# Kernel tuning notes

Measured on AMD Instinct MI355X. Metric: run time of the kernel, lower is better.

The kernel has to match this reference:

```python
import jax, jax.numpy as jnp
import numpy as np

N, T, D, H = 128, 64, 1024, 1024
DA = 4  # spatial dim of feature map


def setup_inputs() -> dict:
    key = jax.random.key(0)
    k1, k2, k3, k4, k5 = jax.random.split(key, 5)
    x = jax.random.normal(k1, (N, T, D), dtype=jnp.float32)
    A = jax.random.normal(k2, (N, H, DA, DA), dtype=jnp.float32)
    Wx = jax.random.normal(k3, (D, 4 * H), dtype=jnp.float32) / np.sqrt(D)
    Wh = jax.random.normal(k4, (H, 4 * H), dtype=jnp.float32) / np.sqrt(H)
    Wattn = jax.random.normal(k5, (H, 4 * H), dtype=jnp.float32) / np.sqrt(H)
    b = jnp.zeros((4 * H,), dtype=jnp.float32)
    return {"x": x, "A": A, "Wx": Wx, "Wh": Wh, "Wattn": Wattn, "b": b}


def _dot_product_attention(prev_h, A_flat):
    # prev_h: (N, H), A_flat: (N, H, L) with L = DA*DA
    scores = jnp.einsum('nh,nhl->nl', prev_h, A_flat) / jnp.sqrt(jnp.float32(H))
    w = jax.nn.softmax(scores, axis=-1)              # (N, L)
    attn = jnp.einsum('nhl,nl->nh', A_flat, w)       # (N, H)
    return attn


def reference(x, A, Wx, Wh, Wattn, b):
    A_flat = A.reshape(A.shape[0], A.shape[1], -1)   # (N, H, L)
    h0 = A.mean(axis=(2, 3))                          # (N, H)
    c0 = h0
    x_t = jnp.swapaxes(x, 0, 1)                       # (T, N, D)

    def step(carry, xt):
        h, c = carry
        attn = _dot_product_attention(h, A_flat)
        a = xt @ Wx + h @ Wh + attn @ Wattn + b       # (N, 4H)
        i, f, o, g = jnp.split(a, 4, axis=1)
        i = jax.nn.sigmoid(i)
        f = jax.nn.sigmoid(f)
        o = jax.nn.sigmoid(o)
        g = jnp.tanh(g)
        c_next = f * c + i * g
        h_next = o * jnp.tanh(c_next)
        return (h_next, c_next), h_next

    _, hn = jax.lax.scan(step, (h0, c0), x_t)         # hn: (T, N, H)
    return jnp.swapaxes(hn, 0, 1)                      # (N, T, H)
```

## Files before the change

### kernel.cpp

```cpp
#include <hip/hip_runtime.h>
#include <stdint.h>
#include <math.h>

typedef __attribute__((ext_vector_type(8))) short short8;
typedef __attribute__((ext_vector_type(4))) short short4v;
typedef __attribute__((ext_vector_type(4))) float f32x4;

__device__ __forceinline__ short f2bf(float f){
  union { float f; uint32_t u; } x; x.f = f;
  uint32_t r = x.u + 0x7fffu + ((x.u >> 16) & 1u);
  return (short)(r >> 16);
}
__device__ __forceinline__ float bf2f(short s){
  union { uint32_t u; float f; } x; x.u = ((uint32_t)(uint16_t)s) << 16;
  return x.f;
}

__device__ __forceinline__ unsigned ld_llc_u32(const void* p){
  return __hip_atomic_load((const unsigned*)p, __ATOMIC_RELAXED, __HIP_MEMORY_SCOPE_AGENT);
}
__device__ __forceinline__ void st_llc_u32(void* p, unsigned v){
  __hip_atomic_store((unsigned*)p, v, __ATOMIC_RELAXED, __HIP_MEMORY_SCOPE_AGENT);
}


__global__ __launch_bounds__(256) void k_wt(const float* __restrict__ Wx,
                                            const float* __restrict__ Wh,
                                            const float* __restrict__ Wattn,
                                            short* __restrict__ W3T){
  __shared__ float tile[64][65];
  int bk = blockIdx.x % 48, bj = blockIdx.x / 48;
  int tx = threadIdx.x & 63, ty = threadIdx.x >> 6;
  int k0 = bk * 64, j0 = bj * 64;
  #pragma unroll
  for (int i = 0; i < 16; ++i){
    int kk = ty * 16 + i;
    int k = k0 + kk;
    const float* src = (k < 1024) ? (Wx + (size_t)k * 4096)
                     : (k < 2048) ? (Wh + (size_t)(k - 1024) * 4096)
                                  : (Wattn + (size_t)(k - 2048) * 4096);
    tile[kk][tx] = src[j0 + tx];
  }
  __syncthreads();
  #pragma unroll
  for (int i = 0; i < 16; ++i){
    int jj = ty * 16 + i;
    W3T[(size_t)(j0 + jj) * 3072 + k0 + tx] = f2bf(tile[tx][jj]);
  }
}

__global__ __launch_bounds__(256) void k_cast(const float* __restrict__ in,
                                              short* __restrict__ out, int n4){
  int i = blockIdx.x * 256 + threadIdx.x;
  if (i >= n4) return;
  float4 v = ((const float4*)in)[i];
  short4v o; o[0] = f2bf(v.x); o[1] = f2bf(v.y); o[2] = f2bf(v.z); o[3] = f2bf(v.w);
  *(short4v*)(out + (size_t)i * 4) = o;
}

__global__ __launch_bounds__(256) void k_castA(const float* __restrict__ A,
                                               short* __restrict__ Abf,
                                               short* __restrict__ Atr){
  const int n = blockIdx.x;
  const int tid = threadIdx.x;
  __shared__ short tile[256][17];
  for (int it = 0; it < 4; ++it){
    int h = it * 256 + tid;
    const float* src = A + ((size_t)n * 1024 + h) * 16;
    short o[16];
    #pragma unroll
    for (int l = 0; l < 16; ++l) o[l] = f2bf(src[l]);
    short8 p0, p1;
    #pragma unroll
    for (int l = 0; l < 8; ++l){ p0[l] = o[l]; p1[l] = o[8 + l]; }
    short8* dst = (short8*)(Abf + ((size_t)n * 1024 + h) * 16);
    dst[0] = p0; dst[1] = p1;
    #pragma unroll
    for (int l = 0; l < 16; ++l) tile[tid][l] = o[l];
    __syncthreads();
    {
      int l = tid >> 4, hc = (tid & 15) * 16;
      short tmp[16];
      #pragma unroll
      for (int k = 0; k < 16; ++k) tmp[k] = tile[hc + k][l];
      short8 q0, q1;
      #pragma unroll
      for (int k = 0; k < 8; ++k){ q0[k] = tmp[k]; q1[k] = tmp[8 + k]; }
      short8* d2 = (short8*)(Atr + (size_t)n * 16384 + l * 1024 + it * 256 + hc);
      d2[0] = q0; d2[1] = q1;
    }
    __syncthreads();
  }
}

__global__ __launch_bounds__(256) void k_init(const float* __restrict__ A,
                                              float* __restrict__ c,
                                              short* __restrict__ hb0,
                                              unsigned* __restrict__ flags){
  int idx = blockIdx.x * 256 + threadIdx.x;
  if (idx < 8192) flags[idx] = 0u;
  const float* p = A + (size_t)idx * 16;
  float s = 0.f;
  #pragma unroll
  for (int l = 0; l < 16; ++l) s += p[l];
  s *= (1.f / 16.f);
  c[idx] = s;
  hb0[idx] = f2bf(s);
}

typedef const __attribute__((address_space(1))) uint32_t* gas1_t;
typedef __attribute__((address_space(3))) uint32_t* las3_t;

__global__ __launch_bounds__(256) void k_xwx(const short* __restrict__ xbf,
                                             const short* __restrict__ W3T,
                                             short* __restrict__ xwx){
  __shared__ short ldsA[128 * 64];
  __shared__ short ldsB[128 * 64];
  const int tid  = threadIdx.x;
  const int lane = tid & 63;
  const int wave = tid >> 6;
  const int orig = blockIdx.x;
  const int wg = (orig & 7) * 256 + (orig >> 3);
  const int n_t = wg >> 6;
  const int m_t = wg & 63;
  const int m0 = m_t * 128;
  const int n0 = n_t * 128;
  const int ra = lane & 15;
  const int q  = lane >> 4;

  f32x4 acc[4][4];
  #pragma unroll
  for (int mf = 0; mf < 4; ++mf)
    #pragma unroll
    for (int jf = 0; jf < 4; ++jf) acc[mf][jf] = f32x4{0.f,0.f,0.f,0.f};

  const int wm = wave >> 1;
  const int wn = wave & 1;

  for (int kt = 0; kt < 16; ++kt){
    const int kb = kt * 64;
    #pragma unroll
    for (int r = 0; r < 4; ++r){
      int id = (wave * 4 + r) * 64 + lane;
      int row = id >> 3, c = id & 7;
      int csrc = c ^ (row & 7);
      const short* src = xbf + (size_t)(m0 + row) * 1024 + kb + csrc * 8;
      short* dst = ldsA + (wave * 4 + r) * 512;
      __builtin_amdgcn_global_load_lds((gas1_t)(const void*)src, (las3_t)(void*)dst, 16, 0, 0);
    }
    #pragma unroll
    for (int r = 0; r < 4; ++r){
      int id = (wave * 4 + r) * 64 + lane;
      int row = id >> 3, c = id & 7;
      int csrc = c ^ (row & 7);
      const short* src = W3T + (size_t)(n0 + row) * 3072 + kb + csrc * 8;
      short* dst = ldsB + (wave * 4 + r) * 512;
      __builtin_amdgcn_global_load_lds((gas1_t)(const void*)src, (las3_t)(void*)dst, 16, 0, 0);
    }
    asm volatile("s_waitcnt vmcnt(0)" ::: "memory");
    __syncthreads();

    #pragma unroll
    for (int kk = 0; kk < 64; kk += 32){
      const int cc = (kk >> 3) + q;
      short8 af[4], bfr[4];
      #pragma unroll
      for (int mf = 0; mf < 4; ++mf){
        int row = wm * 64 + mf * 16 + ra;
        af[mf] = *(const short8*)(ldsA + row * 64 + ((cc ^ (row & 7)) << 3));
      }
      #pragma unroll
      for (int jf = 0; jf < 4; ++jf){
        int row = wn * 64 + jf * 16 + ra;
        bfr[jf] = *(const short8*)(ldsB + row * 64 + ((cc ^ (row & 7)) << 3));
      }
      #pragma unroll
      for (int mf = 0; mf < 4; ++mf)
        #pragma unroll
        for (int jf = 0; jf < 4; ++jf)
          acc[mf][jf] = __builtin_amdgcn_mfma_f32_16x16x32_bf16(af[mf], bfr[jf], acc[mf][jf], 0, 0, 0);
    }
    __syncthreads();
  }

  #pragma unroll
  for (int mf = 0; mf < 4; ++mf)
    #pragma unroll
    for (int jf = 0; jf < 4; ++jf)
      #pragma unroll
      for (int i = 0; i < 4; ++i){
        int row = m0 + wm * 64 + mf * 16 + q * 4 + i;
        int col = n0 + wn * 64 + jf * 16 + ra;
        xwx[(size_t)row * 4096 + col] = f2bf(acc[mf][jf][i]);
      }
}

__global__ __launch_bounds__(256) void k_pw(const short* __restrict__ W3T,
                                            const short* __restrict__ Atr,
                                            short* __restrict__ P){
  const int tid  = threadIdx.x;
  const int lane = tid & 63;
  const int wave = tid >> 6;
  const int blk  = blockIdx.x;
  const int n    = blk >> 4;
  const int jblk = blk & 15;
  const int j0   = jblk * 256 + wave * 64;
  const int ra = lane & 15;
  const int q  = lane >> 4;

  f32x4 acc[4];
  #pragma unroll
  for (int mf = 0; mf < 4; ++mf) acc[mf] = f32x4{0.f,0.f,0.f,0.f};

  auto loadA = [&](int ks, int mf) -> short8 {
    return *(const short8*)(W3T + (size_t)(j0 + mf*16 + ra) * 3072 + 2048 + ks * 32 + q * 8);
  };
  auto loadB = [&](int ks) -> short8 {
    return *(const short8*)(Atr + (size_t)n * 16384 + ra * 1024 + ks * 32 + q * 8);
  };

  short8 aC[4], bC, aN[4], bN;
  #pragma unroll
  for (int mf = 0; mf < 4; ++mf) aC[mf] = loadA(0, mf);
  bC = loadB(0);
  for (int ks = 0; ks < 32; ++ks){
    bool more = (ks + 1) < 32;
    if (more){
      #pragma unroll
      for (int mf = 0; mf < 4; ++mf) aN[mf] = loadA(ks + 1, mf);
      bN = loadB(ks + 1);
    }
    #pragma unroll
    for (int mf = 0; mf < 4; ++mf)
      acc[mf] = __builtin_amdgcn_mfma_f32_16x16x32_bf16(aC[mf], bC, acc[mf], 0, 0, 0);
    if (more){
      #pragma unroll
      for (int mf = 0; mf < 4; ++mf) aC[mf] = aN[mf];
      bC = bN;
    }
  }
  #pragma unroll
  for (int mf = 0; mf < 4; ++mf)
    #pragma unroll
    for (int i = 0; i < 4; ++i){
      int j = j0 + mf * 16 + q * 4 + i;
      P[(size_t)(n * 4096 + j) * 16 + ra] = f2bf(acc[mf][i]);
    }
}

template<int ITERS>
__device__ __forceinline__ void gemm_slice(const short* __restrict__ hRp,
                                           const short* __restrict__ Wl_,
                                           int kbase, int mh, int mf2,
                                           int ra, int q, f32x4 acc[2][2]){
  const int kb8 = kbase >> 3;
  auto loadA = [&](int ks, int m) -> short8 {
    const int k = kbase + ks * 32 + q * 8;
    const int row = mh * 64 + mf2 * 32 + m * 16 + ra;
    return *(const short8*)(hRp + row * 1024 + k);
  };
  auto loadB = [&](int ks, int jf) -> short8 {
    const int kcg = kb8 + ks * 4 + q;
    const int sw = kcg ^ (ra & 7);
    return *(const short8*)(Wl_ + (((jf * 16 + ra) * 128) + sw) * 8);
  };
  short8 Ab[4][2], Bb[2][2];
  Bb[0][0] = loadB(0, 0); Bb[0][1] = loadB(0, 1);
  Bb[1][0] = loadB(1, 0); Bb[1][1] = loadB(1, 1);
  #pragma unroll
  for (int p = 0; p < 4; ++p){ Ab[p][0] = loadA(p, 0); Ab[p][1] = loadA(p, 1); }
  #pragma unroll
  for (int ks = 0; ks < ITERS; ++ks){
    short8 av0 = Ab[ks & 3][0], av1 = Ab[ks & 3][1];
    short8 bv0 = Bb[ks & 1][0], bv1 = Bb[ks & 1][1];
    if (ks + 4 < ITERS){ Ab[ks & 3][0] = loadA(ks + 4, 0); Ab[ks & 3][1] = loadA(ks + 4, 1); }
    if (ks + 2 < ITERS){ Bb[ks & 1][0] = loadB(ks + 2, 0); Bb[ks & 1][1] = loadB(ks + 2, 1); }
    acc[0][0] = __builtin_amdgcn_mfma_f32_16x16x32_bf16(av0, bv0, acc[0][0], 0, 0, 0);
    acc[0][1] = __builtin_amdgcn_mfma_f32_16x16x32_bf16(av0, bv1, acc[0][1], 0, 0, 0);
    acc[1][0] = __builtin_amdgcn_mfma_f32_16x16x32_bf16(av1, bv0, acc[1][0], 0, 0, 0);
    acc[1][1] = __builtin_amdgcn_mfma_f32_16x16x32_bf16(av1, bv1, acc[1][1], 0, 0, 0);
  }
}

__global__ __launch_bounds__(512, 1) void k_loop(
    const short* __restrict__ W3T,
    const short* __restrict__ Abf,
    const short* __restrict__ P,
    short* __restrict__ hbuf,
    float* __restrict__ wbuf,
    const float* __restrict__ cbuf,
    const short* __restrict__ xwx,
    const float* __restrict__ bias,
    float* __restrict__ out,
    unsigned* __restrict__ flags)
{
  __shared__ short Wl[32768];
  __shared__ float part[6][1024];
  __shared__ float fin[2048];
  __shared__ float sred[3][16];
  __shared__ float wlds[64][16];
  __shared__ unsigned lflag[3];

  unsigned* flagsB = flags;
  unsigned* wtag   = flags + 4096;

  const int tid  = threadIdx.x;
  const int lane = tid & 63;
  const int wave = tid >> 6;
  const int bid  = blockIdx.x;
  const int mh   = bid & 1;
  const int jb   = bid >> 1;
  const int u0   = jb * 8;
  const int ra   = lane & 15;
  const int q    = lane >> 4;
  const int mf2  = wave & 1;
  const int kh   = wave >> 1;
  const bool isScore = (bid < 128);
  const int n_s  = mh * 64 + jb;

  #pragma unroll
  for (int it = 0; it < 8; ++it){
    int c16 = it * 512 + tid;
    int jl = c16 >> 7;
    int kc = c16 & 127;
    int jf = jl >> 4, rr = jl & 15;
    int j = (jf * 2 + (rr >> 3)) * 1024 + u0 + (rr & 7);
    short8 v = *(const short8*)(W3T + (size_t)j * 3072 + 1024 + kc * 8);
    int pc = (jf * 16 + rr) * 128 + (kc ^ (rr & 7));
    *(short8*)(Wl + pc * 8) = v;
  }
  if (tid < 3) lflag[tid] = 0u;

  short8 af0[4], af1[4];
  const int st_ = tid - 256;
  const int hh0 = st_ * 4;
  if (wave >= 4 && isScore){
    #pragma unroll
    for (int j = 0; j < 4; ++j){
      const short8* ap = (const short8*)(Abf + ((size_t)n_s * 1024 + hh0 + j) * 16);
      af0[j] = ap[0]; af1[j] = ap[1];
    }
  }

  const int n_loc = tid >> 3, uu = tid & 7;
  const int cn = mh * 64 + n_loc;
  const int cu = u0 + uu;
  float creg = cbuf[(size_t)cn * 1024 + cu];
  const float b0 = bias[cu], b1 = bias[1024 + cu], b2 = bias[2048 + cu], b3 = bias[3072 + cu];
  __syncthreads();

  for (int t = 0; t < 64; ++t){
    const short* hRp = hbuf + (size_t)t * 131072;
    short*       hWp = hbuf + (size_t)(t + 1) * 131072;
    float*       wT  = wbuf + (size_t)t * 4096;

    const short* xp = xwx + ((size_t)cn * 64 + t) * 4096;
    const short xw0 = xp[cu], xw1 = xp[1024 + cu], xw2 = xp[2048 + cu], xw3 = xp[3072 + cu];

    if (t > 0){
      const unsigned tgt = (unsigned)t;
      for (;;){
        unsigned v0 = ld_llc_u32(&flagsB[(mh * 128 + lane * 2)     * 16]);
        unsigned v1 = ld_llc_u32(&flagsB[(mh * 128 + lane * 2 + 1) * 16]);
        unsigned mn = v0 < v1 ? v0 : v1;
        if (__all(mn >= tgt)) break;
        __builtin_amdgcn_s_sleep(1);
      }
    }

    if (isScore && wave >= 4){
      uint64_t hq = *(const uint64_t*)(hRp + n_s * 1024 + hh0);
      float hv[4];
      #pragma unroll
      for (int j = 0; j < 4; ++j) hv[j] = bf2f((short)((hq >> (16 * j)) & 0xffffu));
      float sc[16];
      #pragma unroll
      for (int l = 0; l < 8; ++l){
        float s0 = 0.f, s1 = 0.f;
        #pragma unroll
        for (int j = 0; j < 4; ++j){ s0 += hv[j] * bf2f(af0[j][l]); s1 += hv[j] * bf2f(af1[j][l]); }
        sc[l] = s0; sc[8 + l] = s1;
      }
      #pragma unroll
      for (int off = 1; off < 64; off <<= 1)
        #pragma unroll
        for (int l = 0; l < 16; ++l) sc[l] += __shfl_xor(sc[l], off);
      if (wave > 4){
        if (lane == 0){
          #pragma unroll
          for (int l = 0; l < 16; ++l) sred[wave - 5][l] = sc[l];
          __hip_atomic_store(&lflag[wave - 5], (unsigned)(t + 1),
                             __ATOMIC_RELEASE, __HIP_MEMORY_SCOPE_WORKGROUP);
        }
      } else {
        const unsigned tgt = (unsigned)(t + 1);
        for (;;){
          unsigned a = __hip_atomic_load(&lflag[0], __ATOMIC_ACQUIRE, __HIP_MEMORY_SCOPE_WORKGROUP);
          unsigned b = __hip_atomic_load(&lflag[1], __ATOMIC_ACQUIRE, __HIP_MEMORY_SCOPE_WORKGROUP);
          unsigned c = __hip_atomic_load(&lflag[2], __ATOMIC_ACQUIRE, __HIP_MEMORY_SCOPE_WORKGROUP);
          unsigned mn = a < b ? a : b; mn = c < mn ? c : mn;
          if (mn >= tgt) break;
          __builtin_amdgcn_s_sleep(1);
        }
        float s[16], mx = -1e30f, sum = 0.f;
        #pragma unroll
        for (int l = 0; l < 16; ++l){
          s[l] = (sc[l] + sred[0][l] + sred[1][l] + sred[2][l]) * 0.03125f;
          mx = fmaxf(mx, s[l]);
        }
        #pragma unroll
        for (int l = 0; l < 16; ++l){ s[l] = __expf(s[l] - mx); sum += s[l]; }
        const float inv = 1.f / sum;
        #pragma unroll
        for (int l = 0; l < 16; ++l){
          if (lane == l){
            union { float f; unsigned u; } cv; cv.f = s[l] * inv;
            st_llc_u32(&wT[n_s * 32 + l], cv.u);
          }
        }
        asm volatile("s_waitcnt vmcnt(0)" ::: "memory");
        if (lane == 0) st_llc_u32(&wtag[n_s * 16], (unsigned)(t + 1));
      }
    }

    f32x4 acc[2][2];
    acc[0][0] = f32x4{0.f,0.f,0.f,0.f}; acc[0][1] = f32x4{0.f,0.f,0.f,0.f};
    acc[1][0] = f32x4{0.f,0.f,0.f,0.f}; acc[1][1] = f32x4{0.f,0.f,0.f,0.f};
    if (isScore){
      if      (kh == 0) gemm_slice<10>(hRp, Wl, 0,   mh, mf2, ra, q, acc);
      else if (kh == 1) gemm_slice<10>(hRp, Wl, 320, mh, mf2, ra, q, acc);
      else if (kh == 2) gemm_slice<6> (hRp, Wl, 640, mh, mf2, ra, q, acc);
      else              gemm_slice<6> (hRp, Wl, 832, mh, mf2, ra, q, acc);
    } else {
      if      (kh == 0) gemm_slice<8>(hRp, Wl, 0,   mh, mf2, ra, q, acc);
      else if (kh == 1) gemm_slice<8>(hRp, Wl, 256, mh, mf2, ra, q, acc);
      else if (kh == 2) gemm_slice<8>(hRp, Wl, 512, mh, mf2, ra, q, acc);
      else              gemm_slice<8>(hRp, Wl, 768, mh, mf2, ra, q, acc);
    }

    if (wave >= 2){
      const int pidx = wave - 2;
      #pragma unroll
      for (int m = 0; m < 2; ++m)
        #pragma unroll
        for (int jf = 0; jf < 2; ++jf)
          *(f32x4*)&part[pidx][((m * 2 + jf) * 64 + lane) * 4] = acc[m][jf];
    }
    __syncthreads();

    if (wave < 2){
      #pragma unroll
      for (int m = 0; m < 2; ++m)
        #pragma unroll
        for (int jf = 0; jf < 2; ++jf){
          const int x = ((m * 2 + jf) * 64 + lane) * 4;
          f32x4 s = acc[m][jf];
          s += *(const f32x4*)&part[0 + mf2][x];
          s += *(const f32x4*)&part[2 + mf2][x];
          s += *(const f32x4*)&part[4 + mf2][x];
          const int g = jf * 2 + (ra >> 3);
          const int nl = mf2 * 32 + m * 16 + q * 4;
          #pragma unroll
          for (int i = 0; i < 4; ++i)
            fin[g * 512 + (nl + i) * 8 + (ra & 7)] = s[i];
        }
    }
    if (wave == 6){
      const unsigned tgt = (unsigned)(t + 1);
      for (;;){
        unsigned v = ld_llc_u32(&wtag[(mh * 64 + lane) * 16]);
        if (__all(v >= tgt)) break;
        __builtin_amdgcn_s_sleep(1);
      }
      const f32x4* wp = (const f32x4*)(wbuf + (size_t)t * 4096 + (mh * 64 + lane) * 32);
      f32x4 w0 = wp[0], w1 = wp[1], w2 = wp[2], w3 = wp[3];
      f32x4* wd = (f32x4*)&wlds[lane][0];
      wd[0] = w0; wd[1] = w1; wd[2] = w2; wd[3] = w3;
    }
    __syncthreads();

    float hn;
    {
      float wl[16];
      #pragma unroll
      for (int l = 0; l < 16; ++l) wl[l] = wlds[n_loc][l];
      float pg[4];
      #pragma unroll
      for (int g = 0; g < 4; ++g){
        const short8* pp = (const short8*)(P + ((size_t)cn * 4096 + g * 1024 + cu) * 16);
        short8 pa = pp[0], pb = pp[1];
        float s = 0.f;
        #pragma unroll
        for (int l = 0; l < 8; ++l){ s += bf2f(pa[l]) * wl[l]; s += bf2f(pb[l]) * wl[8 + l]; }
        pg[g] = s;
      }
      const float av = fin[tid]        + bf2f(xw0) + pg[0] + b0;
      const float fv = fin[512 + tid]  + bf2f(xw1) + pg[1] + b1;
      const float ov = fin[1024 + tid] + bf2f(xw2) + pg[2] + b2;
      const float gv = fin[1536 + tid] + bf2f(xw3) + pg[3] + b3;
      const float ig = 1.f / (1.f + __expf(-av));
      const float fg = 1.f / (1.f + __expf(-fv));
      const float og = 1.f / (1.f + __expf(-ov));
      const float gcl = fminf(fmaxf(gv, -20.f), 20.f);
      const float e2g = __expf(2.f * gcl);
      const float gg = (e2g - 1.f) / (e2g + 1.f);
      creg = fg * creg + ig * gg;
      const float ccl = fminf(fmaxf(creg, -20.f), 20.f);
      const float e2c = __expf(2.f * ccl);
      const float th = (e2c - 1.f) / (e2c + 1.f);
      hn = og * th;
      const float hn2 = __shfl_xor(hn, 1);
      if ((tid & 1) == 0){
        unsigned pk = (unsigned)(unsigned short)f2bf(hn)
                    | ((unsigned)(unsigned short)f2bf(hn2) << 16);
        st_llc_u32(hWp + (size_t)cn * 1024 + cu, pk);
      }
    }
    asm volatile("s_waitcnt vmcnt(0)" ::: "memory");
    __syncthreads();
    if (tid == 0 && t < 63) st_llc_u32(&flagsB[(mh * 128 + jb) * 16], (unsigned)(t + 1));
    __builtin_nontemporal_store(hn, &out[((size_t)cn * 64 + t) * 1024 + cu]);
  }
}


extern "C" void kernel_launch(void* const* d_in, const int* in_sizes, int n_in,
                              void* d_out, int out_size, void* d_ws, size_t ws_size,
                              hipStream_t stream)
{
  const float* x     = (const float*)d_in[0];
  const float* A     = (const float*)d_in[1];
  const float* Wx    = (const float*)d_in[2];
  const float* Wh    = (const float*)d_in[3];
  const float* Wattn = (const float*)d_in[4];
  const float* b     = (const float*)d_in[5];
  float* out = (float*)d_out;
  char* ws = (char*)d_ws;

  short*    W3T   = (short*)(ws + 0);
  short*    Abf   = (short*)(ws + 25165824);
  short*    Atr   = (short*)(ws + 29360128);
  short*    xbf   = (short*)(ws + 33554432);
  short*    xwx   = (short*)(ws + 50331648);
  short*    P     = (short*)(ws + 117440512);
  short*    hbuf  = (short*)(ws + 134217728);
  float*    wbuf  = (float*)(ws + 151257088);
  float*    cbuf  = (float*)(ws + 152305664);
  unsigned* flags = (unsigned*)(ws + 152829952);

  hipLaunchKernelGGL(k_wt,    dim3(48 * 64), dim3(256), 0, stream, Wx, Wh, Wattn, W3T);
  hipLaunchKernelGGL(k_cast,  dim3(2097152 / 256), dim3(256), 0, stream, x, xbf, 2097152);
  hipLaunchKernelGGL(k_castA, dim3(128), dim3(256), 0, stream, A, Abf, Atr);
  hipLaunchKernelGGL(k_init,  dim3(512), dim3(256), 0, stream, A, cbuf, hbuf, flags);
  hipLaunchKernelGGL(k_xwx,   dim3(2048), dim3(256), 0, stream, xbf, W3T, xwx);
  hipLaunchKernelGGL(k_pw,    dim3(2048), dim3(256), 0, stream, W3T, Atr, P);
  hipLaunchKernelGGL(k_loop,  dim3(256), dim3(512), 0, stream,
                     W3T, Abf, P, hbuf, wbuf, cbuf, xwx, b, out, flags);
}
```

Measured before the change: 918.1 us.

## Fuse attention scores into h-producer via atomics, drop per-step score phase

Attention scores for the next step are now accumulated by the blocks that produce h, using float atomics into a per-step score buffer striped over four copies. Every block then computes the softmax locally from that buffer. This removes the separate score-wave phase, its intra-block flag handshake, and the second global wtag spin-wait on the serial recurrence critical path. In exchange it adds many global atomic adds per step, which makes the float summation order nondeterministic, plus a zeroing kernel for a larger score buffer.

```diff
diff --git a/kernel.cpp b/kernel.cpp
--- a/kernel.cpp
+++ b/kernel.cpp
@@ -21,6 +21,9 @@
 }
 __device__ __forceinline__ void st_llc_u32(void* p, unsigned v){
   __hip_atomic_store((unsigned*)p, v, __ATOMIC_RELAXED, __HIP_MEMORY_SCOPE_AGENT);
+}
+__device__ __forceinline__ void at_add_llc(float* p, float v){
+  __hip_atomic_fetch_add(p, v, __ATOMIC_RELAXED, __HIP_MEMORY_SCOPE_AGENT);
 }
 
 
@@ -93,19 +96,36 @@
   }
 }
 
+__global__ __launch_bounds__(256) void k_zero(float* __restrict__ sbuf,
+                                              unsigned* __restrict__ flags){
+  int idx = blockIdx.x * 256 + threadIdx.x;
+  if (idx < 532480) sbuf[idx] = 0.f;
+  if (idx < 8192) flags[idx] = 0u;
+}
+
 __global__ __launch_bounds__(256) void k_init(const float* __restrict__ A,
                                               float* __restrict__ c,
                                               short* __restrict__ hb0,
-                                              unsigned* __restrict__ flags){
+                                              float* __restrict__ sbuf){
   int idx = blockIdx.x * 256 + threadIdx.x;
-  if (idx < 8192) flags[idx] = 0u;
+  int n = idx >> 10;
+  const int lane = threadIdx.x & 63;
   const float* p = A + (size_t)idx * 16;
+  float a[16];
   float s = 0.f;
   #pragma unroll
-  for (int l = 0; l < 16; ++l) s += p[l];
+  for (int l = 0; l < 16; ++l){ a[l] = p[l]; s += a[l]; }
   s *= (1.f / 16.f);
   c[idx] = s;
   hb0[idx] = f2bf(s);
+  float sc[16];
+  #pragma unroll
+  for (int l = 0; l < 16; ++l) sc[l] = s * a[l];
+  #pragma unroll
+  for (int off = 1; off < 64; off <<= 1)
+    #pragma unroll
+    for (int l = 0; l < 16; ++l) sc[l] += __shfl_xor(sc[l], off);
+  if (lane < 16) at_add_llc(&sbuf[n * 16 + lane], sc[lane]);
 }
 
 typedef const __attribute__((address_space(1))) uint32_t* gas1_t;
@@ -287,7 +307,7 @@
     const short* __restrict__ Abf,
     const short* __restrict__ P,
     short* __restrict__ hbuf,
-    float* __restrict__ wbuf,
+    float* __restrict__ sbuf,
     const float* __restrict__ cbuf,
     const short* __restrict__ xwx,
     const float* __restrict__ bias,
@@ -297,12 +317,8 @@
   __shared__ short Wl[32768];
   __shared__ float part[6][1024];
   __shared__ float fin[2048];
-  __shared__ float sred[3][16];
-  __shared__ float wlds[64][16];
-  __shared__ unsigned lflag[3];
 
   unsigned* flagsB = flags;
-  unsigned* wtag   = flags + 4096;
 
   const int tid  = threadIdx.x;
   const int lane = tid & 63;
@@ -315,8 +331,6 @@
   const int q    = lane >> 4;
   const int mf2  = wave & 1;
   const int kh   = wave >> 1;
-  const bool isScore = (bid < 128);
-  const int n_s  = mh * 64 + jb;
 
   #pragma unroll
   for (int it = 0; it < 8; ++it){
@@ -329,30 +343,20 @@
     int pc = (jf * 16 + rr) * 128 + (kc ^ (rr & 7));
     *(short8*)(Wl + pc * 8) = v;
   }
-  if (tid < 3) lflag[tid] = 0u;
-
-  short8 af0[4], af1[4];
-  const int st_ = tid - 256;
-  const int hh0 = st_ * 4;
-  if (wave >= 4 && isScore){
-    #pragma unroll
-    for (int j = 0; j < 4; ++j){
-      const short8* ap = (const short8*)(Abf + ((size_t)n_s * 1024 + hh0 + j) * 16);
-      af0[j] = ap[0]; af1[j] = ap[1];
-    }
-  }
 
   const int n_loc = tid >> 3, uu = tid & 7;
   const int cn = mh * 64 + n_loc;
   const int cu = u0 + uu;
   float creg = cbuf[(size_t)cn * 1024 + cu];
   const float b0 = bias[cu], b1 = bias[1024 + cu], b2 = bias[2048 + cu], b3 = bias[3072 + cu];
+  const short8* arp = (const short8*)(Abf + ((size_t)cn * 1024 + cu) * 16);
+  const short8 ar0 = arp[0], ar1 = arp[1];
+  const int scp = jb & 3;
   __syncthreads();
 
   for (int t = 0; t < 64; ++t){
     const short* hRp = hbuf + (size_t)t * 131072;
     short*       hWp = hbuf + (size_t)(t + 1) * 131072;
-    float*       wT  = wbuf + (size_t)t * 4096;
 
     const short* xp = xwx + ((size_t)cn * 64 + t) * 4096;
     const short xw0 = xp[cu], xw1 = xp[1024 + cu], xw2 = xp[2048 + cu], xw3 = xp[3072 + cu];
@@ -368,74 +372,40 @@
       }
     }
 
-    if (isScore && wave >= 4){
-      uint64_t hq = *(const uint64_t*)(hRp + n_s * 1024 + hh0);
-      float hv[4];
-      #pragma unroll
-      for (int j = 0; j < 4; ++j) hv[j] = bf2f((short)((hq >> (16 * j)) & 0xffffu));
-      float sc[16];
-      #pragma unroll
-      for (int l = 0; l < 8; ++l){
-        float s0 = 0.f, s1 = 0.f;
-        #pragma unroll
-        for (int j = 0; j < 4; ++j){ s0 += hv[j] * bf2f(af0[j][l]); s1 += hv[j] * bf2f(af1[j][l]); }
-        sc[l] = s0; sc[8 + l] = s1;
-      }
-      #pragma unroll
-      for (int off = 1; off < 64; off <<= 1)
-        #pragma unroll
-        for (int l = 0; l < 16; ++l) sc[l] += __shfl_xor(sc[l], off);
-      if (wave > 4){
-        if (lane == 0){
-          #pragma unroll
-          for (int l = 0; l < 16; ++l) sred[wave - 5][l] = sc[l];
-          __hip_atomic_store(&lflag[wave - 5], (unsigned)(t + 1),
-                             __ATOMIC_RELEASE, __HIP_MEMORY_SCOPE_WORKGROUP);
-        }
-      } else {
-        const unsigned tgt = (unsigned)(t + 1);
-        for (;;){
-          unsigned a = __hip_atomic_load(&lflag[0], __ATOMIC_ACQUIRE, __HIP_MEMORY_SCOPE_WORKGROUP);
-          unsigned b = __hip_atomic_load(&lflag[1], __ATOMIC_ACQUIRE, __HIP_MEMORY_SCOPE_WORKGROUP);
-          unsigned c = __hip_atomic_load(&lflag[2], __ATOMIC_ACQUIRE, __HIP_MEMORY_SCOPE_WORKGROUP);
-          unsigned mn = a < b ? a : b; mn = c < mn ? c : mn;
-          if (mn >= tgt) break;
-          __builtin_amdgcn_s_sleep(1);
-        }
-        float s[16], mx = -1e30f, sum = 0.f;
-        #pragma unroll
-        for (int l = 0; l < 16; ++l){
-          s[l] = (sc[l] + sred[0][l] + sred[1][l] + sred[2][l]) * 0.03125f;
-          mx = fmaxf(mx, s[l]);
-        }
-        #pragma unroll
-        for (int l = 0; l < 16; ++l){ s[l] = __expf(s[l] - mx); sum += s[l]; }
-        const float inv = 1.f / sum;
-        #pragma unroll
-        for (int l = 0; l < 16; ++l){
-          if (lane == l){
-            union { float f; unsigned u; } cv; cv.f = s[l] * inv;
-            st_llc_u32(&wT[n_s * 32 + l], cv.u);
-          }
-        }
-        asm volatile("s_waitcnt vmcnt(0)" ::: "memory");
-        if (lane == 0) st_llc_u32(&wtag[n_s * 16], (unsigned)(t + 1));
-      }
-    }
-
     f32x4 acc[2][2];
     acc[0][0] = f32x4{0.f,0.f,0.f,0.f}; acc[0][1] = f32x4{0.f,0.f,0.f,0.f};
     acc[1][0] = f32x4{0.f,0.f,0.f,0.f}; acc[1][1] = f32x4{0.f,0.f,0.f,0.f};
-    if (isScore){
-      if      (kh == 0) gemm_slice<10>(hRp, Wl, 0,   mh, mf2, ra, q, acc);
-      else if (kh == 1) gemm_slice<10>(hRp, Wl, 320, mh, mf2, ra, q, acc);
-      else if (kh == 2) gemm_slice<6> (hRp, Wl, 640, mh, mf2, ra, q, acc);
-      else              gemm_slice<6> (hRp, Wl, 832, mh, mf2, ra, q, acc);
-    } else {
-      if      (kh == 0) gemm_slice<8>(hRp, Wl, 0,   mh, mf2, ra, q, acc);
-      else if (kh == 1) gemm_slice<8>(hRp, Wl, 256, mh, mf2, ra, q, acc);
-      else if (kh == 2) gemm_slice<8>(hRp, Wl, 512, mh, mf2, ra, q, acc);
-      else              gemm_slice<8>(hRp, Wl, 768, mh, mf2, ra, q, acc);
+    if      (kh == 0) gemm_slice<8>(hRp, Wl, 0,   mh, mf2, ra, q, acc);
+    else if (kh == 1) gemm_slice<8>(hRp, Wl, 256, mh, mf2, ra, q, acc);
+    else if (kh == 2) gemm_slice<8>(hRp, Wl, 512, mh, mf2, ra, q, acc);
+    else              gemm_slice<8>(hRp, Wl, 768, mh, mf2, ra, q, acc);
+
+    float w[16];
+    {
+      const float* sb = sbuf + (size_t)(t * 4) * 2048 + cn * 16;
+      f32x4 s0 = *(const f32x4*)(sb + 0) ;
+      f32x4 s1 = *(const f32x4*)(sb + 4);
+      f32x4 s2 = *(const f32x4*)(sb + 8);
+      f32x4 s3 = *(const f32x4*)(sb + 12);
+      #pragma unroll
+      for (int cp = 1; cp < 4; ++cp){
+        const float* sc_ = sbuf + (size_t)(t * 4 + cp) * 2048 + cn * 16;
+        s0 += *(const f32x4*)(sc_ + 0);
+        s1 += *(const f32x4*)(sc_ + 4);
+        s2 += *(const f32x4*)(sc_ + 8);
+        s3 += *(const f32x4*)(sc_ + 12);
+      }
+      float sv[16];
+      #pragma unroll
+      for (int i = 0; i < 4; ++i){ sv[i] = s0[i]; sv[4+i] = s1[i]; sv[8+i] = s2[i]; sv[12+i] = s3[i]; }
+      float mx = -1e30f, sum = 0.f;
+      #pragma unroll
+      for (int l = 0; l < 16; ++l){ sv[l] *= 0.03125f; mx = fmaxf(mx, sv[l]); }
+      #pragma unroll
+      for (int l = 0; l < 16; ++l){ sv[l] = __expf(sv[l] - mx); sum += sv[l]; }
+      const float inv = 1.f / sum;
+      #pragma unroll
+      for (int l = 0; l < 16; ++l) w[l] = sv[l] * inv;
     }
 
     if (wave >= 2){
@@ -447,7 +417,6 @@
           *(f32x4*)&part[pidx][((m * 2 + jf) * 64 + lane) * 4] = acc[m][jf];
     }
     __syncthreads();
-
     if (wave < 2){
       #pragma unroll
       for (int m = 0; m < 2; ++m)
@@ -465,25 +434,10 @@
             fin[g * 512 + (nl + i) * 8 + (ra & 7)] = s[i];
         }
     }
-    if (wave == 6){
-      const unsigned tgt = (unsigned)(t + 1);
-      for (;;){
-        unsigned v = ld_llc_u32(&wtag[(mh * 64 + lane) * 16]);
-        if (__all(v >= tgt)) break;
-        __builtin_amdgcn_s_sleep(1);
-      }
-      const f32x4* wp = (const f32x4*)(wbuf + (size_t)t * 4096 + (mh * 64 + lane) * 32);
-      f32x4 w0 = wp[0], w1 = wp[1], w2 = wp[2], w3 = wp[3];
-      f32x4* wd = (f32x4*)&wlds[lane][0];
-      wd[0] = w0; wd[1] = w1; wd[2] = w2; wd[3] = w3;
-    }
     __syncthreads();
 
     float hn;
     {
-      float wl[16];
-      #pragma unroll
-      for (int l = 0; l < 16; ++l) wl[l] = wlds[n_loc][l];
       float pg[4];
       #pragma unroll
       for (int g = 0; g < 4; ++g){
@@ -491,7 +445,7 @@
         short8 pa = pp[0], pb = pp[1];
         float s = 0.f;
         #pragma unroll
-        for (int l = 0; l < 8; ++l){ s += bf2f(pa[l]) * wl[l]; s += bf2f(pb[l]) * wl[8 + l]; }
+        for (int l = 0; l < 8; ++l){ s += bf2f(pa[l]) * w[l]; s += bf2f(pb[l]) * w[8 + l]; }
         pg[g] = s;
       }
       const float av = fin[tid]        + bf2f(xw0) + pg[0] + b0;
@@ -509,11 +463,23 @@
       const float e2c = __expf(2.f * ccl);
       const float th = (e2c - 1.f) / (e2c + 1.f);
       hn = og * th;
-      const float hn2 = __shfl_xor(hn, 1);
-      if ((tid & 1) == 0){
-        unsigned pk = (unsigned)(unsigned short)f2bf(hn)
-                    | ((unsigned)(unsigned short)f2bf(hn2) << 16);
-        st_llc_u32(hWp + (size_t)cn * 1024 + cu, pk);
+      if (t < 63){
+        const float hn2 = __shfl_xor(hn, 1);
+        if ((tid & 1) == 0){
+          unsigned pk = (unsigned)(unsigned short)f2bf(hn)
+                      | ((unsigned)(unsigned short)f2bf(hn2) << 16);
+          st_llc_u32(hWp + (size_t)cn * 1024 + cu, pk);
+        }
+        float v[16];
+        #pragma unroll
+        for (int l = 0; l < 8; ++l){ v[l] = hn * bf2f(ar0[l]); v[8 + l] = hn * bf2f(ar1[l]); }
+        #pragma unroll
+        for (int off = 1; off < 8; off <<= 1)
+          #pragma unroll
+          for (int l = 0; l < 16; ++l) v[l] += __shfl_xor(v[l], off);
+        float* sb = sbuf + (size_t)((t + 1) * 4 + scp) * 2048 + cn * 16;
+        at_add_llc(&sb[uu * 2],     v[uu * 2]);
+        at_add_llc(&sb[uu * 2 + 1], v[uu * 2 + 1]);
       }
     }
     asm volatile("s_waitcnt vmcnt(0)" ::: "memory");
@@ -544,16 +510,17 @@
   short*    xwx   = (short*)(ws + 50331648);
   short*    P     = (short*)(ws + 117440512);
   short*    hbuf  = (short*)(ws + 134217728);
-  float*    wbuf  = (float*)(ws + 151257088);
-  float*    cbuf  = (float*)(ws + 152305664);
-  unsigned* flags = (unsigned*)(ws + 152829952);
+  float*    sbuf  = (float*)(ws + 151257088);
+  float*    cbuf  = (float*)(ws + 153387008);
+  unsigned* flags = (unsigned*)(ws + 153911296);
 
   hipLaunchKernelGGL(k_wt,    dim3(48 * 64), dim3(256), 0, stream, Wx, Wh, Wattn, W3T);
   hipLaunchKernelGGL(k_cast,  dim3(2097152 / 256), dim3(256), 0, stream, x, xbf, 2097152);
   hipLaunchKernelGGL(k_castA, dim3(128), dim3(256), 0, stream, A, Abf, Atr);
-  hipLaunchKernelGGL(k_init,  dim3(512), dim3(256), 0, stream, A, cbuf, hbuf, flags);
+  hipLaunchKernelGGL(k_zero,  dim3(2115), dim3(256), 0, stream, sbuf, flags);
+  hipLaunchKernelGGL(k_init,  dim3(512), dim3(256), 0, stream, A, cbuf, hbuf, sbuf);
   hipLaunchKernelGGL(k_xwx,   dim3(2048), dim3(256), 0, stream, xbf, W3T, xwx);
   hipLaunchKernelGGL(k_pw,    dim3(2048), dim3(256), 0, stream, W3T, Atr, P);
   hipLaunchKernelGGL(k_loop,  dim3(256), dim3(512), 0, stream,
-                     W3T, Abf, P, hbuf, wbuf, cbuf, xwx, b, out, flags);
-}
+                     W3T, Abf, P, hbuf, sbuf, cbuf, xwx, b, out, flags);
+}
```

After: 1.086 ms. 18.3% more time.
